# Performance work log

Hardware: AMD Instinct MI355X
Metric: run time of the kernel (lower is better)

## Reference

```python
import jax, jax.numpy as jnp
import numpy as np

HEADS = 16
HEAD_DIM = 64  # dim // heads = 1024 // 16
SCALE = HEAD_DIM ** -0.5
NEG_INF = -1e30


def setup_inputs() -> dict:
    key = jax.random.key(0)
    ks = jax.random.split(key, 4)
    B, N, D = 4, 2048, 1024
    x = jax.random.normal(ks[0], (B, N, D), dtype=jnp.float32)
    pos_bias = jax.random.normal(ks[1], (HEADS, N, N), dtype=jnp.float32) * 0.02
    w_qkv = jax.random.normal(ks[2], (D, 3 * D), dtype=jnp.float32) * (D ** -0.5)
    w_proj = jax.random.normal(ks[3], (D, D), dtype=jnp.float32) * (D ** -0.5)
    b_proj = jnp.zeros((D,), dtype=jnp.float32)
    return {"x": x, "pos_bias": pos_bias, "w_qkv": w_qkv, "w_proj": w_proj, "b_proj": b_proj}


def reference(x, pos_bias, w_qkv, w_proj, b_proj):
    B, N, D = x.shape
    qkv = x @ w_qkv                                   # [B, N, 3D]
    q, k, v = jnp.split(qkv, 3, axis=-1)
    # '... n (h d) -> ... h n d'
    def to_heads(t):
        return t.reshape(B, N, HEADS, HEAD_DIM).transpose(0, 2, 1, 3)
    q, k, v = to_heads(q), to_heads(k), to_heads(v)
    q = q * SCALE
    sim = jnp.einsum('bhid,bhjd->bhij', q, k)         # [B, H, N, N]
    sim = sim + pos_bias                               # broadcast over batch
    causal = jnp.tril(jnp.ones((N, N), dtype=bool))
    sim = jnp.where(causal, sim, NEG_INF)
    attn = jax.nn.softmax(sim, axis=-1)
    out = jnp.einsum('bhij,bhjd->bhid', attn, v)      # [B, H, N, d]
    out = out.transpose(0, 2, 1, 3).reshape(B, N, HEADS * HEAD_DIM)
    return out @ w_proj + b_proj
```

## Files before the change

### kernel.cpp

```cpp
#include <hip/hip_runtime.h>
#include <hip/hip_bf16.h>
#include <math.h>

typedef __attribute__((ext_vector_type(8))) short bf16x8;
typedef __attribute__((ext_vector_type(4))) float f32x4;
typedef __attribute__((ext_vector_type(8))) unsigned short u16x8;

#define MFMA16(a, b, c) __builtin_amdgcn_mfma_f32_16x16x32_bf16(a, b, c, 0, 0, 0)
#define LOG2E 1.4426950408889634f

__device__ __forceinline__ unsigned short f2b(float f) {
  __hip_bfloat16 h = __float2bfloat16(f);
  return *reinterpret_cast<unsigned short*>(&h);
}

__device__ __forceinline__ uint4 cvt8(const float* __restrict__ p) {
  float4 a = *(const float4*)p;
  float4 b = *(const float4*)(p + 4);
  union {
    unsigned short us[8];
    uint4 u;
  } r;
  r.us[0] = f2b(a.x); r.us[1] = f2b(a.y); r.us[2] = f2b(a.z); r.us[3] = f2b(a.w);
  r.us[4] = f2b(b.x); r.us[5] = f2b(b.y); r.us[6] = f2b(b.z); r.us[7] = f2b(b.w);
  return r.u;
}

__global__ __launch_bounds__(256) void conv_f32_bf16(
    const float* __restrict__ in, unsigned short* __restrict__ out) {
  size_t i = ((size_t)blockIdx.x * 256 + threadIdx.x) * 8;
  *(uint4*)&out[i] = cvt8(in + i);
}

__global__ __launch_bounds__(256) void transpose_f32_bf16(
    const float* __restrict__ in, unsigned short* __restrict__ out, int R,
    int C) {
  __shared__ unsigned short tile[64][72];
  const int tR = blockIdx.y * 64, tC = blockIdx.x * 64;
  const int t = threadIdx.x;
#pragma unroll
  for (int p = 0; p < 4; ++p) {
    int u = t + p * 256, r = u >> 4, c = (u & 15) * 4;
    float4 v = *(const float4*)&in[(size_t)(tR + r) * C + tC + c];
    tile[r][c] = f2b(v.x);
    tile[r][c + 1] = f2b(v.y);
    tile[r][c + 2] = f2b(v.z);
    tile[r][c + 3] = f2b(v.w);
  }
  __syncthreads();
#pragma unroll
  for (int p = 0; p < 2; ++p) {
    int u = t + p * 256, orow = u >> 3, oc = (u & 7) * 8;
    u16x8 v;
#pragma unroll
    for (int e = 0; e < 8; ++e) v[e] = tile[oc + e][orow];
    *(u16x8*)&out[(size_t)(tC + orow) * R + tR + oc] = v;
  }
}

template <int MODE>
__global__ __launch_bounds__(256, 2) void gemm_bt(
    const unsigned short* __restrict__ A, const unsigned short* __restrict__ Bt,
    unsigned short* __restrict__ O0, unsigned short* __restrict__ O1,
    unsigned short* __restrict__ O2, float* __restrict__ OF,
    const float* __restrict__ bias, int K, int N) {
  __shared__ unsigned short sA[128][40];
  __shared__ unsigned short sB[128][40];
  const int m0 = blockIdx.y * 128, n0 = blockIdx.x * 128;
  const int t = threadIdx.x;
  const int wave = t >> 6, lane = t & 63, quad = lane >> 4, t16 = lane & 15;
  const int wr = (wave >> 1) * 64, wc = (wave & 1) * 64;
  const int sr = t >> 2, sc = (t & 3) * 8;

  f32x4 acc[4][4];
#pragma unroll
  for (int i = 0; i < 4; ++i)
#pragma unroll
    for (int j = 0; j < 4; ++j) acc[i][j] = (f32x4){0.f, 0.f, 0.f, 0.f};

  const unsigned short* Ap = A + (size_t)(m0 + sr) * K + sc;
  const unsigned short* Bp = Bt + (size_t)(n0 + sr) * K + sc;
  const size_t rowK64 = (size_t)64 * K;

  for (int k0 = 0; k0 < K; k0 += 32) {
    uint4 a0 = *(const uint4*)(Ap + k0);
    uint4 a1 = *(const uint4*)(Ap + rowK64 + k0);
    uint4 b0 = *(const uint4*)(Bp + k0);
    uint4 b1 = *(const uint4*)(Bp + rowK64 + k0);
    __syncthreads();
    *(uint4*)&sA[sr][sc] = a0;
    *(uint4*)&sA[sr + 64][sc] = a1;
    *(uint4*)&sB[sr][sc] = b0;
    *(uint4*)&sB[sr + 64][sc] = b1;
    __syncthreads();
    bf16x8 af[4], bf[4];
#pragma unroll
    for (int i = 0; i < 4; ++i)
      af[i] = *(const bf16x8*)&sA[wr + i * 16 + t16][quad * 8];
#pragma unroll
    for (int j = 0; j < 4; ++j)
      bf[j] = *(const bf16x8*)&sB[wc + j * 16 + t16][quad * 8];
#pragma unroll
    for (int i = 0; i < 4; ++i)
#pragma unroll
      for (int j = 0; j < 4; ++j) acc[i][j] = MFMA16(af[i], bf[j], acc[i][j]);
  }

#pragma unroll
  for (int i = 0; i < 4; ++i) {
    const int mrow = m0 + wr + i * 16 + quad * 4;
#pragma unroll
    for (int j = 0; j < 4; ++j) {
      const int ncol = n0 + wc + j * 16 + t16;
#pragma unroll
      for (int r = 0; r < 4; ++r) {
        const float v = acc[i][j][r];
        const int mr = mrow + r;
        if (MODE == 0) {
          const int bb = mr >> 11, nn = mr & 2047;
          const int sec = ncol >> 10, rem = ncol & 1023;
          const int hh = rem >> 6, dd = rem & 63;
          const size_t bhh = (size_t)bb * 16 + hh;
          if (sec == 0)
            O0[(bhh * 2048 + nn) * 64 + dd] = f2b(v * (0.125f * LOG2E));
          else if (sec == 1)
            O1[(bhh * 2048 + nn) * 64 + dd] = f2b(v);
          else
            O2[(bhh * 64 + dd) * 2048 + nn] = f2b(v);
        } else {
          OF[(size_t)mr * N + ncol] = v + bias[ncol];
        }
      }
    }
  }
}

__global__ __launch_bounds__(256, 4) void attn_kernel(
    const unsigned short* __restrict__ Q, const unsigned short* __restrict__ Kb,
    const unsigned short* __restrict__ Vt, const float* __restrict__ PB,
    unsigned short* __restrict__ Ao) {
  __shared__ unsigned short sK[64][72];
  __shared__ unsigned short sV[64][72];
  __shared__ unsigned short sQP[64][72];

  const int bh = blockIdx.x & 63;
  const int qt = 31 - (blockIdx.x >> 6);
  const int h = bh & 15;
  const int b = bh >> 4;
  const int q0 = qt * 64;
  const int t = threadIdx.x;
  const int wave = t >> 6, lane = t & 63, quad = lane >> 4, t16 = lane & 15;

  const size_t qbase = ((size_t)bh * 2048 + q0) * 64;
#pragma unroll
  for (int p = 0; p < 2; ++p) {
    int u = t + p * 256, r = u >> 3, c = (u & 7) * 8;
    *(uint4*)&sQP[r][c] = *(const uint4*)&Q[qbase + r * 64 + c];
  }
  __syncthreads();
  const bf16x8 qa0 = *(const bf16x8*)&sQP[wave * 16 + t16][quad * 8];
  const bf16x8 qa1 = *(const bf16x8*)&sQP[wave * 16 + t16][32 + quad * 8];

  f32x4 accO[4];
  float m_r[4], l_r[4];
#pragma unroll
  for (int i = 0; i < 4; ++i) {
    accO[i] = (f32x4){0.f, 0.f, 0.f, 0.f};
    m_r[i] = -INFINITY;
    l_r[i] = 0.f;
  }

  const int qrow = q0 + wave * 16 + quad * 4;
  const int r0 = t >> 3, c0 = (t & 7) * 8;
  const size_t kvrow = (size_t)bh * 2048 * 64;
  const size_t bbase =
      (size_t)h * 4194304 + (size_t)q0 * 2048 + (wave * 16 + quad * 4) * 2048;

  uint4 kv0 = *(const uint4*)&Kb[kvrow + (size_t)r0 * 64 + c0];
  uint4 kv1 = *(const uint4*)&Kb[kvrow + (size_t)(r0 + 32) * 64 + c0];
  uint4 vv0 = *(const uint4*)&Vt[kvrow + (size_t)r0 * 2048 + c0];
  uint4 vv1 = *(const uint4*)&Vt[kvrow + (size_t)(r0 + 32) * 2048 + c0];
  float biasr[4][4];
#pragma unroll
  for (int fc = 0; fc < 4; ++fc)
#pragma unroll
    for (int r = 0; r < 4; ++r)
      biasr[fc][r] = PB[bbase + (size_t)r * 2048 + fc * 16 + t16];

  for (int kt = 0; kt <= qt; ++kt) {
    const int k0 = kt * 64;
    __syncthreads();
    *(uint4*)&sK[r0][c0] = kv0;
    *(uint4*)&sK[r0 + 32][c0] = kv1;
    *(uint4*)&sV[r0][c0] = vv0;
    *(uint4*)&sV[r0 + 32][c0] = vv1;
    __syncthreads();
    if (kt < qt) {
      const size_t nk = (size_t)(k0 + 64);
      kv0 = *(const uint4*)&Kb[kvrow + nk * 64 + (size_t)r0 * 64 + c0];
      kv1 = *(const uint4*)&Kb[kvrow + nk * 64 + (size_t)(r0 + 32) * 64 + c0];
      vv0 = *(const uint4*)&Vt[kvrow + nk + (size_t)r0 * 2048 + c0];
      vv1 = *(const uint4*)&Vt[kvrow + nk + (size_t)(r0 + 32) * 2048 + c0];
    }

    f32x4 s[4];
#pragma unroll
    for (int fc = 0; fc < 4; ++fc) {
      bf16x8 kb0 = *(const bf16x8*)&sK[fc * 16 + t16][quad * 8];
      bf16x8 kb1 = *(const bf16x8*)&sK[fc * 16 + t16][32 + quad * 8];
      f32x4 z = (f32x4){0.f, 0.f, 0.f, 0.f};
      z = MFMA16(qa0, kb0, z);
      z = MFMA16(qa1, kb1, z);
      s[fc] = z;
    }
#pragma unroll
    for (int fc = 0; fc < 4; ++fc)
#pragma unroll
      for (int r = 0; r < 4; ++r) {
        float sv = fmaf(biasr[fc][r], LOG2E, s[fc][r]);
        if (k0 + fc * 16 + t16 > qrow + r) sv = -1e30f;
        s[fc][r] = sv;
      }
    if (kt < qt) {
#pragma unroll
      for (int fc = 0; fc < 4; ++fc)
#pragma unroll
        for (int r = 0; r < 4; ++r)
          biasr[fc][r] =
              PB[bbase + (size_t)r * 2048 + (k0 + 64) + fc * 16 + t16];
    }
    float mx[4];
#pragma unroll
    for (int r = 0; r < 4; ++r)
      mx[r] = fmaxf(fmaxf(s[0][r], s[1][r]), fmaxf(s[2][r], s[3][r]));
#pragma unroll
    for (int off = 1; off < 16; off <<= 1)
#pragma unroll
      for (int r = 0; r < 4; ++r) mx[r] = fmaxf(mx[r], __shfl_xor(mx[r], off));
    float al[4];
#pragma unroll
    for (int r = 0; r < 4; ++r) {
      float mn = fmaxf(m_r[r], mx[r]);
      al[r] = exp2f(m_r[r] - mn);
      m_r[r] = mn;
    }
    float rs[4] = {0.f, 0.f, 0.f, 0.f};
#pragma unroll
    for (int fc = 0; fc < 4; ++fc)
#pragma unroll
      for (int r = 0; r < 4; ++r) {
        float p = exp2f(s[fc][r] - m_r[r]);
        s[fc][r] = p;
        rs[r] += p;
      }
#pragma unroll
    for (int off = 1; off < 16; off <<= 1)
#pragma unroll
      for (int r = 0; r < 4; ++r) rs[r] += __shfl_xor(rs[r], off);
#pragma unroll
    for (int r = 0; r < 4; ++r) l_r[r] = l_r[r] * al[r] + rs[r];
#pragma unroll
    for (int fc = 0; fc < 4; ++fc)
#pragma unroll
      for (int r = 0; r < 4; ++r) accO[fc][r] *= al[r];
#pragma unroll
    for (int fc = 0; fc < 4; ++fc)
#pragma unroll
      for (int r = 0; r < 4; ++r)
        sQP[wave * 16 + quad * 4 + r][fc * 16 + t16] = f2b(s[fc][r]);
    const bf16x8 pa0 = *(const bf16x8*)&sQP[wave * 16 + t16][quad * 8];
    const bf16x8 pa1 = *(const bf16x8*)&sQP[wave * 16 + t16][32 + quad * 8];
#pragma unroll
    for (int fc = 0; fc < 4; ++fc) {
      bf16x8 vb0 = *(const bf16x8*)&sV[fc * 16 + t16][quad * 8];
      bf16x8 vb1 = *(const bf16x8*)&sV[fc * 16 + t16][32 + quad * 8];
      accO[fc] = MFMA16(pa0, vb0, accO[fc]);
      accO[fc] = MFMA16(pa1, vb1, accO[fc]);
    }
  }

  float inv[4];
#pragma unroll
  for (int r = 0; r < 4; ++r) inv[r] = 1.f / l_r[r];
  const size_t obase = (size_t)b * 2048 * 1024 + (size_t)h * 64;
#pragma unroll
  for (int fc = 0; fc < 4; ++fc)
#pragma unroll
    for (int r = 0; r < 4; ++r)
      Ao[obase + (size_t)(q0 + wave * 16 + quad * 4 + r) * 1024 + fc * 16 +
         t16] = f2b(accO[fc][r] * inv[r]);
}

extern "C" void kernel_launch(void* const* d_in, const int* in_sizes, int n_in,
                              void* d_out, int out_size, void* d_ws,
                              size_t ws_size, hipStream_t stream) {
  (void)in_sizes;
  (void)n_in;
  (void)out_size;
  (void)ws_size;
  const float* x = (const float*)d_in[0];
  const float* pb = (const float*)d_in[1];
  const float* wqkv = (const float*)d_in[2];
  const float* wpro = (const float*)d_in[3];
  const float* bpro = (const float*)d_in[4];

  unsigned short* ws = (unsigned short*)d_ws;
  unsigned short* wqkvT = ws;
  unsigned short* wproT = wqkvT + 3072 * 1024;
  unsigned short* Qb = wproT + 1024 * 1024;
  unsigned short* Kb = Qb + 8388608;
  unsigned short* Vtb = Kb + 8388608;
  unsigned short* Ao = Vtb + 8388608;
  unsigned short* xb = Ao;

  conv_f32_bf16<<<4096, 256, 0, stream>>>(x, xb);
  transpose_f32_bf16<<<dim3(48, 16), 256, 0, stream>>>(wqkv, wqkvT, 1024, 3072);
  transpose_f32_bf16<<<dim3(16, 16), 256, 0, stream>>>(wpro, wproT, 1024, 1024);
  gemm_bt<0><<<dim3(24, 64), 256, 0, stream>>>(xb, wqkvT, Qb, Kb, Vtb, nullptr,
                                               nullptr, 1024, 3072);
  attn_kernel<<<2048, 256, 0, stream>>>(Qb, Kb, Vtb, pb, Ao);
  gemm_bt<1><<<dim3(8, 64), 256, 0, stream>>>(Ao, wproT, nullptr, nullptr,
                                              nullptr, (float*)d_out, bpro,
                                              1024, 1024);
}
```

Measured before the change: 583.7 us.

## Transpose score MFMA so each lane owns one query row in attention

The QK^T MFMA operands are swapped, so each lane holds scores for a single query row across four contiguous keys. Row max and row sum then need only two cross-quad shuffles, and the positional-bias loads become contiguous float4 reads. The causal mask is applied only on the diagonal tile, the accumulator rescale is skipped when no row max grows in the wave, and P is written to shared memory as packed bf16 pairs. The cost is extra shuffles to hand the per-row rescale factors and normalizers back into the output accumulator layout.

```diff
diff --git a/kernel.cpp b/kernel.cpp
--- a/kernel.cpp
+++ b/kernel.cpp
@@ -12,6 +12,10 @@
 __device__ __forceinline__ unsigned short f2b(float f) {
   __hip_bfloat16 h = __float2bfloat16(f);
   return *reinterpret_cast<unsigned short*>(&h);
+}
+
+__device__ __forceinline__ unsigned int pk2(float lo, float hi) {
+  return (unsigned int)f2b(lo) | ((unsigned int)f2b(hi) << 16);
 }
 
 __device__ __forceinline__ uint4 cvt8(const float* __restrict__ p) {
@@ -150,6 +154,7 @@
   const int q0 = qt * 64;
   const int t = threadIdx.x;
   const int wave = t >> 6, lane = t & 63, quad = lane >> 4, t16 = lane & 15;
+  const int kloc = quad * 4;
 
   const size_t qbase = ((size_t)bh * 2048 + q0) * 64;
 #pragma unroll
@@ -162,30 +167,24 @@
   const bf16x8 qa1 = *(const bf16x8*)&sQP[wave * 16 + t16][32 + quad * 8];
 
   f32x4 accO[4];
-  float m_r[4], l_r[4];
-#pragma unroll
-  for (int i = 0; i < 4; ++i) {
-    accO[i] = (f32x4){0.f, 0.f, 0.f, 0.f};
-    m_r[i] = -INFINITY;
-    l_r[i] = 0.f;
-  }
-
-  const int qrow = q0 + wave * 16 + quad * 4;
+#pragma unroll
+  for (int i = 0; i < 4; ++i) accO[i] = (f32x4){0.f, 0.f, 0.f, 0.f};
+  float m = -INFINITY, l = 0.f;
+
+  const int qrow = q0 + wave * 16 + t16;
   const int r0 = t >> 3, c0 = (t & 7) * 8;
   const size_t kvrow = (size_t)bh * 2048 * 64;
-  const size_t bbase =
-      (size_t)h * 4194304 + (size_t)q0 * 2048 + (wave * 16 + quad * 4) * 2048;
+  const float* pbp =
+      PB + (size_t)h * 4194304 + (size_t)qrow * 2048 + kloc;
 
   uint4 kv0 = *(const uint4*)&Kb[kvrow + (size_t)r0 * 64 + c0];
   uint4 kv1 = *(const uint4*)&Kb[kvrow + (size_t)(r0 + 32) * 64 + c0];
   uint4 vv0 = *(const uint4*)&Vt[kvrow + (size_t)r0 * 2048 + c0];
   uint4 vv1 = *(const uint4*)&Vt[kvrow + (size_t)(r0 + 32) * 2048 + c0];
-  float biasr[4][4];
-#pragma unroll
-  for (int fc = 0; fc < 4; ++fc)
-#pragma unroll
-    for (int r = 0; r < 4; ++r)
-      biasr[fc][r] = PB[bbase + (size_t)r * 2048 + fc * 16 + t16];
+  f32x4 biasf[4];
+#pragma unroll
+  for (int fr = 0; fr < 4; ++fr)
+    biasf[fr] = *(const f32x4*)&pbp[fr * 16];
 
   for (int kt = 0; kt <= qt; ++kt) {
     const int k0 = kt * 64;
@@ -205,69 +204,80 @@
 
     f32x4 s[4];
 #pragma unroll
-    for (int fc = 0; fc < 4; ++fc) {
-      bf16x8 kb0 = *(const bf16x8*)&sK[fc * 16 + t16][quad * 8];
-      bf16x8 kb1 = *(const bf16x8*)&sK[fc * 16 + t16][32 + quad * 8];
+    for (int fr = 0; fr < 4; ++fr) {
+      bf16x8 kb0 = *(const bf16x8*)&sK[fr * 16 + t16][quad * 8];
+      bf16x8 kb1 = *(const bf16x8*)&sK[fr * 16 + t16][32 + quad * 8];
       f32x4 z = (f32x4){0.f, 0.f, 0.f, 0.f};
-      z = MFMA16(qa0, kb0, z);
-      z = MFMA16(qa1, kb1, z);
-      s[fc] = z;
-    }
-#pragma unroll
-    for (int fc = 0; fc < 4; ++fc)
+      z = MFMA16(kb0, qa0, z);
+      z = MFMA16(kb1, qa1, z);
+      s[fr] = z;
+    }
+#pragma unroll
+    for (int fr = 0; fr < 4; ++fr)
+#pragma unroll
+      for (int r = 0; r < 4; ++r)
+        s[fr][r] = fmaf(biasf[fr][r], LOG2E, s[fr][r]);
+    if (kt == qt) {
+#pragma unroll
+      for (int fr = 0; fr < 4; ++fr)
+#pragma unroll
+        for (int r = 0; r < 4; ++r)
+          if (k0 + fr * 16 + kloc + r > qrow) s[fr][r] = -1e30f;
+    }
+    if (kt < qt) {
+#pragma unroll
+      for (int fr = 0; fr < 4; ++fr)
+        biasf[fr] = *(const f32x4*)&pbp[k0 + 64 + fr * 16];
+    }
+
+    float mxa = fmaxf(fmaxf(s[0][0], s[0][1]), fmaxf(s[0][2], s[0][3]));
+    float mxb = fmaxf(fmaxf(s[1][0], s[1][1]), fmaxf(s[1][2], s[1][3]));
+    float mxc = fmaxf(fmaxf(s[2][0], s[2][1]), fmaxf(s[2][2], s[2][3]));
+    float mxd = fmaxf(fmaxf(s[3][0], s[3][1]), fmaxf(s[3][2], s[3][3]));
+    float mx = fmaxf(fmaxf(mxa, mxb), fmaxf(mxc, mxd));
+    mx = fmaxf(mx, __shfl_xor(mx, 16));
+    mx = fmaxf(mx, __shfl_xor(mx, 32));
+
+    float al = 1.f;
+    const bool grow = __any(mx > m) != 0;
+    if (grow) {
+      const float mn = fmaxf(m, mx);
+      al = exp2f(m - mn);
+      m = mn;
+    }
+    float rsa = 0.f, rsb = 0.f;
+#pragma unroll
+    for (int fr = 0; fr < 4; ++fr) {
+      float p0 = exp2f(s[fr][0] - m);
+      float p1 = exp2f(s[fr][1] - m);
+      float p2 = exp2f(s[fr][2] - m);
+      float p3 = exp2f(s[fr][3] - m);
+      s[fr][0] = p0; s[fr][1] = p1; s[fr][2] = p2; s[fr][3] = p3;
+      rsa += p0 + p1;
+      rsb += p2 + p3;
+    }
+    float rs = rsa + rsb;
+    rs += __shfl_xor(rs, 16);
+    rs += __shfl_xor(rs, 32);
+    l = fmaf(l, al, rs);
+    if (grow) {
 #pragma unroll
       for (int r = 0; r < 4; ++r) {
-        float sv = fmaf(biasr[fc][r], LOG2E, s[fc][r]);
-        if (k0 + fc * 16 + t16 > qrow + r) sv = -1e30f;
-        s[fc][r] = sv;
+        const float alr = __shfl(al, (lane & 48) + kloc + r);
+        accO[0][r] *= alr;
+        accO[1][r] *= alr;
+        accO[2][r] *= alr;
+        accO[3][r] *= alr;
       }
-    if (kt < qt) {
-#pragma unroll
-      for (int fc = 0; fc < 4; ++fc)
-#pragma unroll
-        for (int r = 0; r < 4; ++r)
-          biasr[fc][r] =
-              PB[bbase + (size_t)r * 2048 + (k0 + 64) + fc * 16 + t16];
-    }
-    float mx[4];
-#pragma unroll
-    for (int r = 0; r < 4; ++r)
-      mx[r] = fmaxf(fmaxf(s[0][r], s[1][r]), fmaxf(s[2][r], s[3][r]));
-#pragma unroll
-    for (int off = 1; off < 16; off <<= 1)
-#pragma unroll
-      for (int r = 0; r < 4; ++r) mx[r] = fmaxf(mx[r], __shfl_xor(mx[r], off));
-    float al[4];
-#pragma unroll
-    for (int r = 0; r < 4; ++r) {
-      float mn = fmaxf(m_r[r], mx[r]);
-      al[r] = exp2f(m_r[r] - mn);
-      m_r[r] = mn;
-    }
-    float rs[4] = {0.f, 0.f, 0.f, 0.f};
-#pragma unroll
-    for (int fc = 0; fc < 4; ++fc)
-#pragma unroll
-      for (int r = 0; r < 4; ++r) {
-        float p = exp2f(s[fc][r] - m_r[r]);
-        s[fc][r] = p;
-        rs[r] += p;
-      }
-#pragma unroll
-    for (int off = 1; off < 16; off <<= 1)
-#pragma unroll
-      for (int r = 0; r < 4; ++r) rs[r] += __shfl_xor(rs[r], off);
-#pragma unroll
-    for (int r = 0; r < 4; ++r) l_r[r] = l_r[r] * al[r] + rs[r];
-#pragma unroll
-    for (int fc = 0; fc < 4; ++fc)
-#pragma unroll
-      for (int r = 0; r < 4; ++r) accO[fc][r] *= al[r];
-#pragma unroll
-    for (int fc = 0; fc < 4; ++fc)
-#pragma unroll
-      for (int r = 0; r < 4; ++r)
-        sQP[wave * 16 + quad * 4 + r][fc * 16 + t16] = f2b(s[fc][r]);
+    }
+
+#pragma unroll
+    for (int fr = 0; fr < 4; ++fr) {
+      uint2 pv;
+      pv.x = pk2(s[fr][0], s[fr][1]);
+      pv.y = pk2(s[fr][2], s[fr][3]);
+      *(uint2*)&sQP[wave * 16 + t16][fr * 16 + kloc] = pv;
+    }
     const bf16x8 pa0 = *(const bf16x8*)&sQP[wave * 16 + t16][quad * 8];
     const bf16x8 pa1 = *(const bf16x8*)&sQP[wave * 16 + t16][32 + quad * 8];
 #pragma unroll
@@ -279,16 +289,17 @@
     }
   }
 
-  float inv[4];
-#pragma unroll
-  for (int r = 0; r < 4; ++r) inv[r] = 1.f / l_r[r];
+  const float inv = 1.f / l;
+  float invr[4];
+#pragma unroll
+  for (int r = 0; r < 4; ++r) invr[r] = __shfl(inv, (lane & 48) + kloc + r);
   const size_t obase = (size_t)b * 2048 * 1024 + (size_t)h * 64;
 #pragma unroll
   for (int fc = 0; fc < 4; ++fc)
 #pragma unroll
     for (int r = 0; r < 4; ++r)
       Ao[obase + (size_t)(q0 + wave * 16 + quad * 4 + r) * 1024 + fc * 16 +
-         t16] = f2b(accO[fc][r] * inv[r]);
+         t16] = f2b(accO[fc][r] * invr[r]);
 }
 
 extern "C" void kernel_launch(void* const* d_in, const int* in_sizes, int n_in,
```

Result: no change. 586.7 us (+0.5%).
